# Optimization experiments

Measured on AMD Instinct MI355X. Metric: run time of the kernel, lower is better.

## Reference

```python
import jax, jax.numpy as jnp
import numpy as np


def setup_inputs() -> dict:
    key = jax.random.key(0)
    kq, kk, kv = jax.random.split(key, 3)
    B, L, S, H, E, D = 2, 2048, 2048, 16, 64, 64
    return {
        "queries": jax.random.normal(kq, (B, L, H, E), dtype=jnp.float32),
        "keys": jax.random.normal(kk, (B, S, H, E), dtype=jnp.float32),
        "values": jax.random.normal(kv, (B, S, H, D), dtype=jnp.float32),
    }


def reference(queries, keys, values):
    # FullAttention forward (mask_flag=False, dropout=0.0 -> identity)
    E = queries.shape[-1]
    scale = 1.0 / jnp.sqrt(jnp.asarray(E, dtype=queries.dtype))
    # scores: [B, H, L, S]
    scores = jnp.einsum('blhe,bshe->bhls', queries, keys)
    A = jax.nn.softmax(scale * scores, axis=-1)
    # output: [B, L, H, D]
    V = jnp.einsum('bhls,bshd->blhd', A, values)
    return V
```

## Files before the change

kernel.cpp:

```cpp
#include <hip/hip_runtime.h>
#include <hip/hip_bf16.h>
#include <string.h>


#define NB 2
#define LL 2048
#define SS 2048
#define HH 16
#define EE 64
#define DD 64
#define KVB 64
#define NT (SS / KVB)
#define NWG2 (NB * HH * (LL / 64))

typedef _Float16 f16x8 __attribute__((ext_vector_type(8)));
typedef float f32x4 __attribute__((ext_vector_type(4)));
typedef float f32x16 __attribute__((ext_vector_type(16)));
typedef unsigned uint2v __attribute__((ext_vector_type(2)));
typedef unsigned uint4v __attribute__((ext_vector_type(4)));
typedef const __attribute__((address_space(1))) void* gas_p;
typedef __attribute__((address_space(3))) void* las_p;

__device__ __forceinline__ unsigned pk2h(float a, float b) {
    auto h = __builtin_amdgcn_cvt_pkrtz(a, b);
    unsigned u;
    __builtin_memcpy(&u, &h, 4);
    return u;
}

__device__ __forceinline__ float fexp2(float x) {
#if defined(__has_builtin) && __has_builtin(__builtin_amdgcn_exp2f)
    return __builtin_amdgcn_exp2f(x);
#else
    return exp2f(x);
#endif
}

__device__ __forceinline__ void gll16(const void* g, void* l) {
    __builtin_amdgcn_global_load_lds((gas_p)g, (las_p)l, 16, 0, 0);
}

__device__ __forceinline__ uint2v plswap(unsigned a, unsigned b) {
#if defined(__has_builtin) && __has_builtin(__builtin_amdgcn_permlane32_swap)
    return __builtin_amdgcn_permlane32_swap(a, b, false, false);
#else
    unsigned ax = (unsigned)__shfl_xor((int)a, 32);
    unsigned bx = (unsigned)__shfl_xor((int)b, 32);
    int l32 = (int)(threadIdx.x & 32);
    uint2v r;
    r[0] = l32 ? bx : a;
    r[1] = l32 ? b : ax;
    return r;
#endif
}

__device__ __forceinline__ float fbits(unsigned u) {
    float f; __builtin_memcpy(&f, &u, 4); return f;
}
__device__ __forceinline__ unsigned ubits(float f) {
    unsigned u; __builtin_memcpy(&u, &f, 4); return u;
}
__device__ __forceinline__ float xsum32(float x) {
    uint2v r = plswap(ubits(x), ubits(x));
    return fbits(r[0]) + fbits(r[1]);
}

__global__ __launch_bounds__(256) void prepKV(const float* __restrict__ K,
                                              const float* __restrict__ V,
                                              unsigned short* __restrict__ Kh,
                                              unsigned short* __restrict__ Vth) {
    const int NTILE = NB * HH * NT;
    const bool isV = blockIdx.x >= NTILE;
    const int tile = blockIdx.x & (NTILE - 1);
    const int it = tile & (NT - 1);
    const int bh = tile >> 5;
    const int b = bh >> 4, h = bh & 15;
    const int t = threadIdx.x;

    if (!isV) {
        const int s = t >> 2, ec = t & 3;
        const float* src = K + (((size_t)b * SS + it * KVB + s) * HH + h) * EE + ec * 16;
        f32x4 x0 = ((const f32x4*)src)[0];
        f32x4 x1 = ((const f32x4*)src)[1];
        f32x4 x2 = ((const f32x4*)src)[2];
        f32x4 x3 = ((const f32x4*)src)[3];
        uint4v c0, c1;
        c0.x = pk2h(x0[0], x0[1]); c0.y = pk2h(x0[2], x0[3]);
        c0.z = pk2h(x1[0], x1[1]); c0.w = pk2h(x1[2], x1[3]);
        c1.x = pk2h(x2[0], x2[1]); c1.y = pk2h(x2[2], x2[3]);
        c1.z = pk2h(x3[0], x3[1]); c1.w = pk2h(x3[2], x3[3]);
        char* dst = (char*)Kh + (size_t)tile * 8192;
        const int sw = (s & 7) << 4;
        *(uint4v*)(dst + ((s * 128 + ec * 32) ^ sw)) = c0;
        *(uint4v*)(dst + ((s * 128 + ec * 32 + 16) ^ sw)) = c1;
    } else {
        __shared__ float Vt[64 * 68];
        {
            const int s = t >> 2, dc = t & 3;
            const float* src = V + (((size_t)b * SS + it * KVB + s) * HH + h) * DD + dc * 16;
            f32x4 x0 = ((const f32x4*)src)[0];
            f32x4 x1 = ((const f32x4*)src)[1];
            f32x4 x2 = ((const f32x4*)src)[2];
            f32x4 x3 = ((const f32x4*)src)[3];
            float* row = Vt + s * 68 + dc * 16;
            ((f32x4*)row)[0] = x0; ((f32x4*)row)[1] = x1;
            ((f32x4*)row)[2] = x2; ((f32x4*)row)[3] = x3;
        }
        __syncthreads();
        {
            const int d = t >> 2, sc = t & 3;
            float w[16];
#pragma unroll
            for (int j = 0; j < 16; ++j) w[j] = Vt[(sc * 16 + j) * 68 + d];
            uint4v c0, c1;
            c0.x = pk2h(w[0], w[1]); c0.y = pk2h(w[2], w[3]);
            c0.z = pk2h(w[4], w[5]); c0.w = pk2h(w[6], w[7]);
            c1.x = pk2h(w[8], w[9]); c1.y = pk2h(w[10], w[11]);
            c1.z = pk2h(w[12], w[13]); c1.w = pk2h(w[14], w[15]);
            char* dst = (char*)Vth + (size_t)tile * 8192;
            const int sw = (d & 7) << 4;
            *(uint4v*)(dst + ((d * 128 + sc * 32) ^ sw)) = c0;
            *(uint4v*)(dst + ((d * 128 + sc * 32 + 16) ^ sw)) = c1;
        }
    }
}

__global__ __launch_bounds__(256, 4) void fattn11(const unsigned short* __restrict__ Kh,
                                                  const unsigned short* __restrict__ Vth,
                                                  const float* __restrict__ Q,
                                                  float* __restrict__ O) {
    __shared__ __align__(16) char LB[16640];
    __shared__ float lsh[4][32];
    char* KA = LB;
    char* KB = LB + 8192;

    const int tid = threadIdx.x;
    const int lane = tid & 63;
    const int wid = tid >> 6;
    const int ln = lane & 31;
    const int hi = lane >> 5;
    const int qg = wid >> 1;
    const int sh = wid & 1;

    const int bid0 = blockIdx.x;
    const int bid = (bid0 & 7) * (NWG2 >> 3) + (bid0 >> 3);
    const int bh = bid >> 5;
    const int qt = bid & 31;
    const int b = bh >> 4, h = bh & 15;
    const int qrow = qt * 64 + qg * 32 + ln;

    const float qs = 0.125f * 1.44269504088896340736f;
    const float* qptr = Q + (((size_t)b * LL + qrow) * HH + h) * EE + hi * 8;
    f16x8 qf[4];
#pragma unroll
    for (int ks = 0; ks < 4; ++ks) {
        f32x4 a0 = *(const f32x4*)(qptr + ks * 16);
        f32x4 a1 = *(const f32x4*)(qptr + ks * 16 + 4);
        union { f16x8 v; unsigned u[4]; } cv;
        cv.u[0] = pk2h(a0[0] * qs, a0[1] * qs);
        cv.u[1] = pk2h(a0[2] * qs, a0[3] * qs);
        cv.u[2] = pk2h(a1[0] * qs, a1[1] * qs);
        cv.u[3] = pk2h(a1[2] * qs, a1[3] * qs);
        qf[ks] = cv.v;
    }

    f32x16 o0, o1;
    f32x16 zs;
#pragma unroll
    for (int i = 0; i < 16; ++i) { o0[i] = 0.f; o1[i] = 0.f; zs[i] = 0.f; }
    float l = 0.f;

    const char* Kg = (const char*)Kh + (size_t)bh * (NT * 8192);
    const char* Vg = (const char*)Vth + (size_t)bh * (NT * 8192);

    auto STAGE_K = [&](int it, char* Ks) {
        const size_t off = (size_t)it * 8192 + wid * 2048 + lane * 16;
        gll16(Kg + off, Ks + wid * 2048);
        gll16(Kg + off + 1024, Ks + wid * 2048 + 1024);
    };

    const int swz = (ln & 7) << 4;
    const int srow = sh * 32 + ln;
    const int vcol = sh * 64;
    const int vo00 = (ln * 128 + vcol + hi * 16) ^ swz;
    const int vo01 = ((32 + ln) * 128 + vcol + hi * 16) ^ swz;
    const int vo10 = (ln * 128 + vcol + 32 + hi * 16) ^ swz;
    const int vo11 = ((32 + ln) * 128 + vcol + 32 + hi * 16) ^ swz;

    auto COMPUTE = [&](const char* Ks, const char* vtile) {
        f16x8 v00 = *(const f16x8*)(vtile + vo00);
        f16x8 v01 = *(const f16x8*)(vtile + vo01);
        f16x8 v10 = *(const f16x8*)(vtile + vo10);
        f16x8 v11 = *(const f16x8*)(vtile + vo11);

        f16x8 k0 = *(const f16x8*)(Ks + ((srow * 128 + 0 * 32 + hi * 16) ^ swz));
        f16x8 k1 = *(const f16x8*)(Ks + ((srow * 128 + 1 * 32 + hi * 16) ^ swz));
        f16x8 k2 = *(const f16x8*)(Ks + ((srow * 128 + 2 * 32 + hi * 16) ^ swz));
        f16x8 k3 = *(const f16x8*)(Ks + ((srow * 128 + 3 * 32 + hi * 16) ^ swz));
        __builtin_amdgcn_s_setprio(1);
        f32x16 st = __builtin_amdgcn_mfma_f32_32x32x16_f16(k0, qf[0], zs, 0, 0, 0);
        st = __builtin_amdgcn_mfma_f32_32x32x16_f16(k1, qf[1], st, 0, 0, 0);
        st = __builtin_amdgcn_mfma_f32_32x32x16_f16(k2, qf[2], st, 0, 0, 0);
        st = __builtin_amdgcn_mfma_f32_32x32x16_f16(k3, qf[3], st, 0, 0, 0);
        __builtin_amdgcn_s_setprio(0);

        float t0 = 0.f, t1 = 0.f, t2 = 0.f, t3 = 0.f;
#pragma unroll
        for (int r = 0; r < 16; r += 4) {
            st[r] = fexp2(st[r]);
            st[r + 1] = fexp2(st[r + 1]);
            st[r + 2] = fexp2(st[r + 2]);
            st[r + 3] = fexp2(st[r + 3]);
            t0 += st[r]; t1 += st[r + 1]; t2 += st[r + 2]; t3 += st[r + 3];
        }
        l += (t0 + t1) + (t2 + t3);

        {
            uint2v r0 = plswap(pk2h(st[0], st[1]), pk2h(st[4], st[5]));
            uint2v r1 = plswap(pk2h(st[2], st[3]), pk2h(st[6], st[7]));
            union { f16x8 v; unsigned u[4]; } w;
            w.u[0] = r0[0]; w.u[1] = r1[0]; w.u[2] = r0[1]; w.u[3] = r1[1];
            __builtin_amdgcn_s_setprio(1);
            o0 = __builtin_amdgcn_mfma_f32_32x32x16_f16(v00, w.v, o0, 0, 0, 0);
            o1 = __builtin_amdgcn_mfma_f32_32x32x16_f16(v01, w.v, o1, 0, 0, 0);
            __builtin_amdgcn_s_setprio(0);
        }
        {
            uint2v r2 = plswap(pk2h(st[8], st[9]), pk2h(st[12], st[13]));
            uint2v r3 = plswap(pk2h(st[10], st[11]), pk2h(st[14], st[15]));
            union { f16x8 v; unsigned u[4]; } w;
            w.u[0] = r2[0]; w.u[1] = r3[0]; w.u[2] = r2[1]; w.u[3] = r3[1];
            __builtin_amdgcn_s_setprio(1);
            o0 = __builtin_amdgcn_mfma_f32_32x32x16_f16(v10, w.v, o0, 0, 0, 0);
            o1 = __builtin_amdgcn_mfma_f32_32x32x16_f16(v11, w.v, o1, 0, 0, 0);
            __builtin_amdgcn_s_setprio(0);
        }
    };

    STAGE_K(0, KA);
    __syncthreads();
    for (int t = 0; t < NT; t += 2) {
        if (t + 1 < NT) STAGE_K(t + 1, KB);
        COMPUTE(KA, Vg + (size_t)t * 8192);
        __syncthreads();
        if (t + 2 < NT) STAGE_K(t + 2, KA);
        COMPUTE(KB, Vg + (size_t)(t + 1) * 8192);
        __syncthreads();
    }

    l = xsum32(l);
    if (hi == 0) lsh[wid][ln] = l;
    __syncthreads();
    const float lo = lsh[wid ^ 1][ln];
    const float lstar = l + lo;

    float* pbuf = (float*)LB + qg * (32 * 65);
    if (sh == 1) {
#pragma unroll
        for (int r = 0; r < 16; ++r) {
            const int d = (r & 3) + 8 * (r >> 2) + 4 * hi;
            pbuf[ln * 65 + d] = o0[r];
            pbuf[ln * 65 + 32 + d] = o1[r];
        }
    }
    __syncthreads();
    if (sh == 0) {
        const float invl = 1.f / lstar;
        float* optr = O + (((size_t)b * LL + qrow) * HH + h) * DD;
#pragma unroll
        for (int t = 0; t < 4; ++t) {
            f32x4 w0, w1;
#pragma unroll
            for (int i = 0; i < 4; ++i) {
                const int d = t * 8 + hi * 4 + i;
                w0[i] = (o0[4 * t + i] + pbuf[ln * 65 + d]) * invl;
                w1[i] = (o1[4 * t + i] + pbuf[ln * 65 + 32 + d]) * invl;
            }
            *(f32x4*)(optr + t * 8 + hi * 4) = w0;
            *(f32x4*)(optr + 32 + t * 8 + hi * 4) = w1;
        }
    }
}

typedef unsigned u2f __attribute__((ext_vector_type(2)));
__global__ __launch_bounds__(256) void fattn1(const float* __restrict__ Q,
                                              const float* __restrict__ K,
                                              const float* __restrict__ V,
                                              float* __restrict__ O) {
    __shared__ __align__(16) short Klds[KVB * 64];
    __shared__ __align__(16) short Vtlds[64 * KVB];
    __shared__ __align__(16) short Plds[4][16 * 64];

    const int tid = threadIdx.x;
    const int lane = tid & 63;
    const int wid = tid >> 6;
    const int g = (lane >> 4) & 3;
    const int c = lane & 15;

    const int bid = blockIdx.x;
    const int bh = bid >> 5;
    const int qt = bid & 31;
    const int b = bh >> 4;
    const int h = bh & 15;
    const int q0 = qt * 64;

    const int qrow = q0 + wid * 16 + c;
    const float* qptr = Q + (((size_t)b * LL + qrow) * HH + h) * EE;
    const float qs = 0.125f * 1.44269504088896340736f;
    f16x8 qf[2];
#pragma unroll
    for (int kk = 0; kk < 2; ++kk) {
        f32x4 a0 = *(const f32x4*)(qptr + kk * 32 + g * 8);
        f32x4 a1 = *(const f32x4*)(qptr + kk * 32 + g * 8 + 4);
        union { f16x8 v; unsigned u[4]; } cv;
        cv.u[0] = pk2h(a0[0] * qs, a0[1] * qs);
        cv.u[1] = pk2h(a0[2] * qs, a0[3] * qs);
        cv.u[2] = pk2h(a1[0] * qs, a1[1] * qs);
        cv.u[3] = pk2h(a1[2] * qs, a1[3] * qs);
        qf[kk] = cv.v;
    }

    f32x4 osacc[4];
    const f32x4 fzero = {0.f, 0.f, 0.f, 0.f};
#pragma unroll
    for (int i = 0; i < 4; ++i) osacc[i] = fzero;
    float m_run = -1e30f;
    float l_run = 0.f;

    const int km = tid & 15;
    const int kr = tid >> 4;

    for (int it = 0; it < NT; ++it) {
        const int s_glob = it * KVB;
        f32x4 kreg[4];
#pragma unroll
        for (int p = 0; p < 4; ++p) {
            int s = kr + p * 16;
            kreg[p] = *(const f32x4*)(K + (((size_t)b * SS + s_glob + s) * HH + h) * EE + km * 4);
        }
        f32x4 vreg[4];
#pragma unroll
        for (int p = 0; p < 4; ++p) {
            int s = kr * 4 + p;
            vreg[p] = *(const f32x4*)(V + (((size_t)b * SS + s_glob + s) * HH + h) * DD + km * 4);
        }
        __syncthreads();
#pragma unroll
        for (int p = 0; p < 4; ++p) {
            int s = kr + p * 16;
            u2f w;
            w.x = pk2h(kreg[p][0], kreg[p][1]);
            w.y = pk2h(kreg[p][2], kreg[p][3]);
            int byte = (s * 128 + km * 8) ^ ((s & 7) << 4);
            *(u2f*)((char*)Klds + byte) = w;
        }
#pragma unroll
        for (int i = 0; i < 4; ++i) {
            int d = km * 4 + i;
            u2f w;
            w.x = pk2h(vreg[0][i], vreg[1][i]);
            w.y = pk2h(vreg[2][i], vreg[3][i]);
            int byte = (d * 128 + kr * 8) ^ ((d & 7) << 4);
            *(u2f*)((char*)Vtlds + byte) = w;
        }
        __syncthreads();

        f32x4 stv[4];
#pragma unroll
        for (int fr = 0; fr < 4; ++fr) stv[fr] = fzero;
#pragma unroll
        for (int fr = 0; fr < 4; ++fr) {
            int s = fr * 16 + c;
            f16x8 kf0 = *(const f16x8*)((const char*)Klds + ((s * 128 + 16 * g) ^ ((s & 7) << 4)));
            stv[fr] = __builtin_amdgcn_mfma_f32_16x16x32_f16(kf0, qf[0], stv[fr], 0, 0, 0);
            f16x8 kf1 = *(const f16x8*)((const char*)Klds + ((s * 128 + 64 + 16 * g) ^ ((s & 7) << 4)));
            stv[fr] = __builtin_amdgcn_mfma_f32_16x16x32_f16(kf1, qf[1], stv[fr], 0, 0, 0);
        }

        float pmax = stv[0][0];
#pragma unroll
        for (int fr = 0; fr < 4; ++fr)
#pragma unroll
            for (int r = 0; r < 4; ++r) pmax = fmaxf(pmax, stv[fr][r]);
        pmax = fmaxf(pmax, __shfl_xor(pmax, 16));
        pmax = fmaxf(pmax, __shfl_xor(pmax, 32));
        float mnew = fmaxf(m_run, pmax);
        float alpha = fexp2(m_run - mnew);
        float tsum = 0.f;
#pragma unroll
        for (int fr = 0; fr < 4; ++fr)
#pragma unroll
            for (int r = 0; r < 4; ++r) {
                float e = fexp2(stv[fr][r] - mnew);
                stv[fr][r] = e;
                tsum += e;
            }
        tsum += __shfl_xor(tsum, 16);
        tsum += __shfl_xor(tsum, 32);
        l_run = l_run * alpha + tsum;
        m_run = mnew;
#pragma unroll
        for (int fr = 0; fr < 4; ++fr)
#pragma unroll
            for (int r = 0; r < 4; ++r) osacc[fr][r] *= alpha;

        short* plb = &Plds[wid][0];
#pragma unroll
        for (int fr = 0; fr < 4; ++fr) {
            u2f w;
            w.x = pk2h(stv[fr][0], stv[fr][1]);
            w.y = pk2h(stv[fr][2], stv[fr][3]);
            int byte = (c * 128 + fr * 32 + g * 8) ^ ((c & 7) << 4);
            *(u2f*)((char*)plb + byte) = w;
        }
        f16x8 pb0 = *(const f16x8*)((const char*)plb + ((c * 128 + 16 * g) ^ ((c & 7) << 4)));
        f16x8 pb1 = *(const f16x8*)((const char*)plb + ((c * 128 + 64 + 16 * g) ^ ((c & 7) << 4)));

#pragma unroll
        for (int fr = 0; fr < 4; ++fr) {
            int d = fr * 16 + c;
            f16x8 vf0 = *(const f16x8*)((const char*)Vtlds + ((d * 128 + 16 * g) ^ ((d & 7) << 4)));
            osacc[fr] = __builtin_amdgcn_mfma_f32_16x16x32_f16(vf0, pb0, osacc[fr], 0, 0, 0);
            f16x8 vf1 = *(const f16x8*)((const char*)Vtlds + ((d * 128 + 64 + 16 * g) ^ ((d & 7) << 4)));
            osacc[fr] = __builtin_amdgcn_mfma_f32_16x16x32_f16(vf1, pb1, osacc[fr], 0, 0, 0);
        }
    }

    float invl = 1.f / l_run;
    float* optr = O + (((size_t)b * LL + qrow) * HH + h) * DD;
#pragma unroll
    for (int fr = 0; fr < 4; ++fr) {
        f32x4 o;
        o[0] = osacc[fr][0] * invl;
        o[1] = osacc[fr][1] * invl;
        o[2] = osacc[fr][2] * invl;
        o[3] = osacc[fr][3] * invl;
        *(f32x4*)(optr + fr * 16 + g * 4) = o;
    }
}

extern "C" void kernel_launch(void* const* d_in, const int* in_sizes, int n_in,
                              void* d_out, int out_size, void* d_ws, size_t ws_size,
                              hipStream_t stream) {
    const float* Q = (const float*)d_in[0];
    const float* K = (const float*)d_in[1];
    const float* V = (const float*)d_in[2];
    float* Op = (float*)d_out;

    const size_t halfBytes = (size_t)NB * HH * SS * EE * 2;
    if (ws_size >= 2 * halfBytes) {
        unsigned short* Kht = (unsigned short*)d_ws;
        unsigned short* Vht = (unsigned short*)((char*)d_ws + halfBytes);
        hipLaunchKernelGGL(prepKV, dim3(2 * NB * HH * NT), dim3(256), 0, stream, K, V, Kht, Vht);
        hipLaunchKernelGGL(fattn11, dim3(NWG2), dim3(256), 0, stream, Kht, Vht, Q, Op);
    } else {
        hipLaunchKernelGGL(fattn1, dim3(NB * HH * (LL / 64)), dim3(256), 0, stream, Q, K, V, Op);
    }
}
```

Baseline: 65.42 us.

## Give each wave private double-buffered K tiles and drop block-wide barriers

Each wave now stages its own 32-row half of the K tile into a private LDS double buffer and synchronises with a per-wave vmcnt wait instead of block-wide __syncthreads. The goal is to remove cross-wave barrier stalls in the main loop. The cost is duplicated K loads across the two query-group waves, which share the same half, and LDS per block grows from about 16KB to 32KB, which may lower occupancy. It also relies on the async global-to-LDS copy being visible after only a vmcnt wait with no barrier.

```diff
diff --git a/kernel.cpp b/kernel.cpp
--- a/kernel.cpp
+++ b/kernel.cpp
@@ -125,14 +125,12 @@
     }
 }
 
-__global__ __launch_bounds__(256, 4) void fattn11(const unsigned short* __restrict__ Kh,
+__global__ __launch_bounds__(256, 4) void fattn14(const unsigned short* __restrict__ Kh,
                                                   const unsigned short* __restrict__ Vth,
                                                   const float* __restrict__ Q,
                                                   float* __restrict__ O) {
-    __shared__ __align__(16) char LB[16640];
+    __shared__ __align__(16) char LB[32768];
     __shared__ float lsh[4][32];
-    char* KA = LB;
-    char* KB = LB + 8192;
 
     const int tid = threadIdx.x;
     const int lane = tid & 63;
@@ -148,6 +146,9 @@
     const int qt = bid & 31;
     const int b = bh >> 4, h = bh & 15;
     const int qrow = qt * 64 + qg * 32 + ln;
+
+    char* kb0 = LB + wid * 8192;
+    char* kb1 = LB + wid * 8192 + 4096;
 
     const float qs = 0.125f * 1.44269504088896340736f;
     const float* qptr = Q + (((size_t)b * LL + qrow) * HH + h) * EE + hi * 8;
@@ -165,40 +166,58 @@
     }
 
     f32x16 o0, o1;
-    f32x16 zs;
-#pragma unroll
-    for (int i = 0; i < 16; ++i) { o0[i] = 0.f; o1[i] = 0.f; zs[i] = 0.f; }
+#pragma unroll
+    for (int i = 0; i < 16; ++i) { o0[i] = 0.f; o1[i] = 0.f; }
     float l = 0.f;
 
-    const char* Kg = (const char*)Kh + (size_t)bh * (NT * 8192);
+    const char* Kg = (const char*)Kh + (size_t)bh * (NT * 8192) + sh * 4096;
     const char* Vg = (const char*)Vth + (size_t)bh * (NT * 8192);
 
-    auto STAGE_K = [&](int it, char* Ks) {
-        const size_t off = (size_t)it * 8192 + wid * 2048 + lane * 16;
-        gll16(Kg + off, Ks + wid * 2048);
-        gll16(Kg + off + 1024, Ks + wid * 2048 + 1024);
-    };
-
     const int swz = (ln & 7) << 4;
-    const int srow = sh * 32 + ln;
     const int vcol = sh * 64;
     const int vo00 = (ln * 128 + vcol + hi * 16) ^ swz;
     const int vo01 = ((32 + ln) * 128 + vcol + hi * 16) ^ swz;
     const int vo10 = (ln * 128 + vcol + 32 + hi * 16) ^ swz;
     const int vo11 = ((32 + ln) * 128 + vcol + 32 + hi * 16) ^ swz;
-
-    auto COMPUTE = [&](const char* Ks, const char* vtile) {
+    const int lk0 = (ln * 128 + 0 * 32 + hi * 16) ^ swz;
+    const int lk1 = (ln * 128 + 1 * 32 + hi * 16) ^ swz;
+    const int lk2 = (ln * 128 + 2 * 32 + hi * 16) ^ swz;
+    const int lk3 = (ln * 128 + 3 * 32 + hi * 16) ^ swz;
+
+    auto STAGE_K = [&](int it, char* kb) {
+        const char* src = Kg + (size_t)it * 8192 + lane * 16;
+        gll16(src, kb);
+        gll16(src + 1024, kb + 1024);
+        gll16(src + 2048, kb + 2048);
+        gll16(src + 3072, kb + 3072);
+    };
+
+    STAGE_K(0, kb0);
+
+    for (int t = 0; t < NT; ++t) {
+        char* kcur = (t & 1) ? kb1 : kb0;
+        char* knext = (t & 1) ? kb0 : kb1;
+
+        asm volatile("s_waitcnt vmcnt(0)" ::: "memory");
+        __builtin_amdgcn_sched_barrier(0);
+
+        const char* vtile = Vg + (size_t)t * 8192;
         f16x8 v00 = *(const f16x8*)(vtile + vo00);
         f16x8 v01 = *(const f16x8*)(vtile + vo01);
         f16x8 v10 = *(const f16x8*)(vtile + vo10);
         f16x8 v11 = *(const f16x8*)(vtile + vo11);
-
-        f16x8 k0 = *(const f16x8*)(Ks + ((srow * 128 + 0 * 32 + hi * 16) ^ swz));
-        f16x8 k1 = *(const f16x8*)(Ks + ((srow * 128 + 1 * 32 + hi * 16) ^ swz));
-        f16x8 k2 = *(const f16x8*)(Ks + ((srow * 128 + 2 * 32 + hi * 16) ^ swz));
-        f16x8 k3 = *(const f16x8*)(Ks + ((srow * 128 + 3 * 32 + hi * 16) ^ swz));
+        if (t + 1 < NT) STAGE_K(t + 1, knext);
+        __builtin_amdgcn_sched_barrier(0);
+
+        f16x8 k0 = *(const f16x8*)(kcur + lk0);
+        f16x8 k1 = *(const f16x8*)(kcur + lk1);
+        f16x8 k2 = *(const f16x8*)(kcur + lk2);
+        f16x8 k3 = *(const f16x8*)(kcur + lk3);
+        f32x16 st;
+#pragma unroll
+        for (int i = 0; i < 16; ++i) st[i] = 0.f;
         __builtin_amdgcn_s_setprio(1);
-        f32x16 st = __builtin_amdgcn_mfma_f32_32x32x16_f16(k0, qf[0], zs, 0, 0, 0);
+        st = __builtin_amdgcn_mfma_f32_32x32x16_f16(k0, qf[0], st, 0, 0, 0);
         st = __builtin_amdgcn_mfma_f32_32x32x16_f16(k1, qf[1], st, 0, 0, 0);
         st = __builtin_amdgcn_mfma_f32_32x32x16_f16(k2, qf[2], st, 0, 0, 0);
         st = __builtin_amdgcn_mfma_f32_32x32x16_f16(k3, qf[3], st, 0, 0, 0);
@@ -235,17 +254,6 @@
             o1 = __builtin_amdgcn_mfma_f32_32x32x16_f16(v11, w.v, o1, 0, 0, 0);
             __builtin_amdgcn_s_setprio(0);
         }
-    };
-
-    STAGE_K(0, KA);
-    __syncthreads();
-    for (int t = 0; t < NT; t += 2) {
-        if (t + 1 < NT) STAGE_K(t + 1, KB);
-        COMPUTE(KA, Vg + (size_t)t * 8192);
-        __syncthreads();
-        if (t + 2 < NT) STAGE_K(t + 2, KA);
-        COMPUTE(KB, Vg + (size_t)(t + 1) * 8192);
-        __syncthreads();
     }
 
     l = xsum32(l);
@@ -452,7 +460,7 @@
         unsigned short* Kht = (unsigned short*)d_ws;
         unsigned short* Vht = (unsigned short*)((char*)d_ws + halfBytes);
         hipLaunchKernelGGL(prepKV, dim3(2 * NB * HH * NT), dim3(256), 0, stream, K, V, Kht, Vht);
-        hipLaunchKernelGGL(fattn11, dim3(NWG2), dim3(256), 0, stream, Kht, Vht, Q, Op);
+        hipLaunchKernelGGL(fattn14, dim3(NWG2), dim3(256), 0, stream, Kht, Vht, Q, Op);
     } else {
         hipLaunchKernelGGL(fattn1, dim3(NB * HH * (LL / 64)), dim3(256), 0, stream, Q, K, V, Op);
     }
```

Result: slower. 72.90 us (+11.4%).
